# Kernel optimization log

Measured on AMD Instinct MI355X. Metric: run time of the kernel, lower is better.

Reference implementation:

```python
import jax, jax.numpy as jnp
import numpy as np

D_MODEL = 1024
PATCH = 16
HID = 256
VOCAB = 256

def setup_inputs() -> dict:
    key = jax.random.key(0)
    ks = jax.random.split(key, 12)
    B, N = 16, 512
    s = lambda *sh: 1.0 / np.sqrt(sh[-1])
    inp = {
        'latents': jax.random.normal(ks[0], (B, N, D_MODEL), dtype=jnp.float32),
        'target_bytes': jax.random.randint(ks[1], (B, N * PATCH), 0, VOCAB, dtype=jnp.int64),
        'W_proj': jax.random.normal(ks[2], (HID, D_MODEL), dtype=jnp.float32) * s(HID, D_MODEL),
        'b_proj': jnp.zeros((HID,), dtype=jnp.float32),
        'emb_table': jax.random.normal(ks[3], (VOCAB, HID), dtype=jnp.float32),
        'W_ih': jax.random.normal(ks[4], (3 * HID, 2 * HID), dtype=jnp.float32) * s(1, 2 * HID),
        'W_hh': jax.random.normal(ks[5], (3 * HID, HID), dtype=jnp.float32) * s(1, HID),
        'b_ih': jnp.zeros((3 * HID,), dtype=jnp.float32),
        'b_hh': jnp.zeros((3 * HID,), dtype=jnp.float32),
        'W_head': jax.random.normal(ks[6], (VOCAB, HID), dtype=jnp.float32) * s(VOCAB, HID),
        'b_head': jnp.zeros((VOCAB,), dtype=jnp.float32),
    }
    return inp

def _gru_scan(x_proj, W_hh, b_hh, h0):
    # x_proj: [T, BN, 3H] precomputed input projections (incl. b_ih)
    def step(h, xg):
        hg = h @ W_hh.T + b_hh                      # [BN, 3H]
        xr, xz, xn = jnp.split(xg, 3, axis=-1)
        hr, hz, hn = jnp.split(hg, 3, axis=-1)
        r = jax.nn.sigmoid(xr + hr)
        z = jax.nn.sigmoid(xz + hz)
        n = jnp.tanh(xn + r * hn)
        h_new = (1.0 - z) * n + z * h
        return h_new, h_new
    _, outs = jax.lax.scan(step, h0, x_proj)
    return outs                                      # [T, BN, H]

def reference(latents, target_bytes, W_proj, b_proj, emb_table, W_ih, W_hh, b_ih, b_hh, W_head, b_head):
    B, N, D = latents.shape
    BN = B * N
    latent_ctx = (latents.reshape(BN, D) @ W_proj.T + b_proj)        # [BN, H]
    targets = target_bytes.reshape(BN, PATCH)
    sos = jnp.zeros((BN, 1), dtype=targets.dtype)
    rnn_in_bytes = jnp.concatenate([sos, targets[:, :-1]], axis=1)   # [BN, P]
    emb = emb_table[rnn_in_bytes]                                    # [BN, P, H]
    lat_exp = jnp.broadcast_to(latent_ctx[:, None, :], (BN, PATCH, HID))
    rnn_input = jnp.concatenate([emb, lat_exp], axis=-1)             # [BN, P, 2H]
    x_proj = jnp.einsum('bpi,gi->bpg', rnn_input, W_ih) + b_ih       # [BN, P, 3H]
    h0 = jnp.zeros((BN, HID), dtype=latents.dtype)
    outs = _gru_scan(jnp.swapaxes(x_proj, 0, 1), W_hh, b_hh, h0)     # [P, BN, H]
    outs = jnp.swapaxes(outs, 0, 1)                                  # [BN, P, H]
    logits = jnp.einsum('bph,vh->bpv', outs, W_head) + b_head        # [BN, P, 256]
    return logits.reshape(B, N, PATCH, VOCAB)
```

## Files before the change

kernel.cpp:

```cpp
#include <hip/hip_runtime.h>
#include <math.h>

#define NSEQ 8192
#define PATCHL 16
#define HIDN 256
#define VOCABN 256

typedef __attribute__((ext_vector_type(4))) float f32x4;
typedef __attribute__((ext_vector_type(8))) short bf16x8;

__device__ __forceinline__ unsigned short f2bf(float f) {
    unsigned int x = __float_as_uint(f);
    unsigned int r = (x + 0x7fffu + ((x >> 16) & 1u)) >> 16;
    return (unsigned short)r;
}
__device__ __forceinline__ float bf2f(unsigned short b) {
    return __uint_as_float(((unsigned int)b) << 16);
}
__device__ __forceinline__ float sigf(float x)   { return 1.f / (1.f + __expf(-x)); }
__device__ __forceinline__ float tanhf_(float x) { return 2.f / (1.f + __expf(-2.f * x)) - 1.f; }

__global__ __launch_bounds__(256)
void pack_frag(const float* __restrict__ src, int ld, int col0, int nks,
               unsigned short* __restrict__ dst)
{
    const int g = blockIdx.x * 256 + threadIdx.x;
    const int lane = g & 63;
    const int ks = (g / 64) % nks;
    const int T  = g / (64 * nks);
    const float* s = src + (size_t)(T * 16 + (lane & 15)) * ld + col0 + ks * 32 + ((lane >> 4) & 3) * 8;
    unsigned int q[4];
#pragma unroll
    for (int j = 0; j < 4; j++) {
        unsigned int lo = f2bf(s[2 * j]);
        unsigned int hi = f2bf(s[2 * j + 1]);
        q[j] = lo | (hi << 16);
    }
    uint4 v; v.x = q[0]; v.y = q[1]; v.z = q[2]; v.w = q[3];
    *(uint4*)(dst + (size_t)g * 8) = v;
}

template<bool ASRC_BF16, int OUT_MODE>
__global__ __launch_bounds__(512)
void gemm_mfma(const void* __restrict__ Asrc, int lda,
               const unsigned short* __restrict__ bpack, int nks_total,
               const float* __restrict__ bias, void* __restrict__ Cdst, int ldc,
               int K)
{
    const int tid = threadIdx.x;
    const int w = tid >> 6, lane = tid & 63;
    const int l15 = lane & 15, kg = (lane >> 4) & 3;
    const int bm = blockIdx.x * 128, bn = blockIdx.y * 64;

    __shared__ unsigned short As[2][128 * 64];

    const int srow = tid >> 2;
    const int scol = (tid & 3) * 16;
    const int nkt = K / 64;

    f32x4 acc[4];
#pragma unroll
    for (int nt = 0; nt < 4; nt++) acc[nt] = 0.f;

    const int wb0 = srow * 128 + ((scol * 2) ^ ((srow & 7) << 4));
    const int wb1 = srow * 128 + ((scol * 2 + 16) ^ ((srow & 7) << 4));

#define STAGE(kt, buf) do {                                                         \
        const int gk = (kt) * 64 + scol;                                            \
        unsigned short tmp[16];                                                     \
        if (ASRC_BF16) {                                                            \
            const unsigned short* A = (const unsigned short*)Asrc;                  \
            *(uint4*)(tmp)     = *(const uint4*)(A + (size_t)(bm + srow) * lda + gk);      \
            *(uint4*)(tmp + 8) = *(const uint4*)(A + (size_t)(bm + srow) * lda + gk + 8);  \
        } else {                                                                    \
            const float* A = (const float*)Asrc;                                    \
            const float4 a0 = *(const float4*)(A + (size_t)(bm + srow) * lda + gk);       \
            const float4 a1 = *(const float4*)(A + (size_t)(bm + srow) * lda + gk + 4);   \
            const float4 a2 = *(const float4*)(A + (size_t)(bm + srow) * lda + gk + 8);   \
            const float4 a3 = *(const float4*)(A + (size_t)(bm + srow) * lda + gk + 12);  \
            tmp[0] = f2bf(a0.x);  tmp[1] = f2bf(a0.y);  tmp[2] = f2bf(a0.z);  tmp[3] = f2bf(a0.w);   \
            tmp[4] = f2bf(a1.x);  tmp[5] = f2bf(a1.y);  tmp[6] = f2bf(a1.z);  tmp[7] = f2bf(a1.w);   \
            tmp[8] = f2bf(a2.x);  tmp[9] = f2bf(a2.y);  tmp[10] = f2bf(a2.z); tmp[11] = f2bf(a2.w);  \
            tmp[12] = f2bf(a3.x); tmp[13] = f2bf(a3.y); tmp[14] = f2bf(a3.z); tmp[15] = f2bf(a3.w);  \
        }                                                                           \
        *(uint4*)((char*)As[buf] + wb0) = *(uint4*)tmp;                             \
        *(uint4*)((char*)As[buf] + wb1) = *(uint4*)(tmp + 8);                       \
    } while (0)

    STAGE(0, 0);
    __syncthreads();

    for (int kt = 0; kt < nkt; ++kt) {
        if (kt + 1 < nkt) STAGE(kt + 1, (kt + 1) & 1);
        const unsigned short* buf = As[kt & 1];
        const int row = w * 16 + l15;
#pragma unroll
        for (int ks = 0; ks < 2; ++ks) {
            const int bo = row * 128 + (((ks * 64) + kg * 16) ^ ((row & 7) << 4));
            const bf16x8 a = *(const bf16x8*)((const char*)buf + bo);
#pragma unroll
            for (int nt = 0; nt < 4; ++nt) {
                const int T = blockIdx.y * 4 + nt;
                const bf16x8 b = *(const bf16x8*)(bpack + (((size_t)T * nks_total + (kt * 2 + ks)) * 64 + lane) * 8);
                acc[nt] = __builtin_amdgcn_mfma_f32_16x16x32_bf16(a, b, acc[nt], 0, 0, 0);
            }
        }
        __syncthreads();
    }
#undef STAGE

#pragma unroll
    for (int nt = 0; nt < 4; ++nt) {
        const int n = bn + nt * 16 + l15;
        const float bv = bias ? bias[n] : 0.f;
#pragma unroll
        for (int rr = 0; rr < 4; ++rr) {
            const int m = bm + w * 16 + kg * 4 + rr;
            const float v = acc[nt][rr] + bv;
            if (OUT_MODE == 0)      ((float*)Cdst)[(size_t)m * ldc + n] = v;
            else if (OUT_MODE == 1) ((unsigned short*)Cdst)[(size_t)m * ldc + n] = f2bf(v);
            else                    ((unsigned short*)Cdst)[(size_t)m * 1024 + (n & 255) * 4 + (n >> 8)] = f2bf(v);
        }
    }
}

#define G4S 1032
__global__ __launch_bounds__(512)
void gru_scan_fused(const int* __restrict__ bytes,
                    const unsigned short* __restrict__ latg4,
                    const unsigned short* __restrict__ pmx4,
                    const unsigned short* __restrict__ wpack,
                    const float* __restrict__ b_hh,
                    unsigned short* __restrict__ hh,
                    int seq0)
{
    const int tid  = threadIdx.x;
    const int w    = tid >> 6;
    const int lane = tid & 63;
    const int l15  = lane & 15;
    const int kg   = (lane >> 4) & 3;
    const int s0l  = blockIdx.x * 16;
    const int s0g  = seq0 + s0l;

    __shared__ unsigned short PMs[16 * G4S];
    __shared__ unsigned short LG[16 * G4S];
    __shared__ unsigned short H[16 * 256];
    __shared__ int BYs[256];

    if (tid < 256) BYs[tid] = bytes[(size_t)s0g * PATCHL + tid];

#pragma unroll
    for (int j = 0; j < 4; ++j) {
        const int idx = j * 512 + tid;
        const int row = idx >> 7, col = idx & 127;
        *(uint4*)(LG + row * G4S + col * 8) =
            *(const uint4*)(latg4 + (size_t)(s0g + row) * 1024 + col * 8);
    }

    float bhr[2], bhz[2], bhn[2];
#pragma unroll
    for (int nt = 0; nt < 2; nt++) {
        const int u = w * 32 + nt * 16 + l15;
        bhr[nt] = b_hh[u]; bhz[nt] = b_hh[256 + u]; bhn[nt] = b_hh[512 + u];
    }

    float hreg[2][4];
#pragma unroll
    for (int nt = 0; nt < 2; nt++)
#pragma unroll
        for (int rr = 0; rr < 4; rr++) hreg[nt][rr] = 0.f;

    __syncthreads();

    for (int p = 0; p < PATCHL; ++p) {
#pragma unroll
        for (int j = 0; j < 4; ++j) {
            const int idx = j * 512 + tid;
            const int row = idx >> 7, col = idx & 127;
            const int bv = p ? BYs[row * PATCHL + p - 1] : 0;
            *(uint4*)(PMs + row * G4S + col * 8) =
                *(const uint4*)(pmx4 + (size_t)bv * 1024 + col * 8);
        }

        if (p) {
#pragma unroll
            for (int rj = 0; rj < 2; ++rj) {
                const int row = w * 2 + rj;
                const int boff = (lane * 8) ^ ((row & 7) << 4);
                const ushort4 v = *(const ushort4*)((const char*)(H + row * 256) + boff);
                *(ushort4*)(hh + ((size_t)(s0l + row) * PATCHL + (p - 1)) * 256 + lane * 4) = v;
            }
        }

        f32x4 accr[2], accz[2], accn[2];
#pragma unroll
        for (int nt = 0; nt < 2; nt++) { accr[nt] = 0.f; accz[nt] = 0.f; accn[nt] = 0.f; }
        if (p != 0) {
#pragma unroll
            for (int ks = 0; ks < 8; ++ks) {
                const int s = l15;
                const int off = (ks * 64 + kg * 16) ^ ((s & 7) << 4);
                const bf16x8 a = *(const bf16x8*)(H + s * 256 + (off >> 1));
#pragma unroll
                for (int nt = 0; nt < 2; nt++) {
                    const int tb = w * 2 + nt;
                    const bf16x8 br = *(const bf16x8*)(wpack + (((size_t)(tb)      * 8 + ks) * 64 + lane) * 8);
                    const bf16x8 bz = *(const bf16x8*)(wpack + (((size_t)(16 + tb) * 8 + ks) * 64 + lane) * 8);
                    const bf16x8 bn = *(const bf16x8*)(wpack + (((size_t)(32 + tb) * 8 + ks) * 64 + lane) * 8);
                    accr[nt] = __builtin_amdgcn_mfma_f32_16x16x32_bf16(a, br, accr[nt], 0, 0, 0);
                    accz[nt] = __builtin_amdgcn_mfma_f32_16x16x32_bf16(a, bz, accz[nt], 0, 0, 0);
                    accn[nt] = __builtin_amdgcn_mfma_f32_16x16x32_bf16(a, bn, accn[nt], 0, 0, 0);
                }
            }
        }
        __syncthreads();

#pragma unroll
        for (int nt = 0; nt < 2; nt++) {
            const int u = w * 32 + nt * 16 + l15;
#pragma unroll
            for (int rr = 0; rr < 4; rr++) {
                const int sl = kg * 4 + rr;
                const ushort4 pm4 = *(const ushort4*)(PMs + sl * G4S + u * 4);
                const ushort4 lg4 = *(const ushort4*)(LG  + sl * G4S + u * 4);
                const float xr = bf2f(lg4.x) + bf2f(pm4.x) + bhr[nt];
                const float xz = bf2f(lg4.y) + bf2f(pm4.y) + bhz[nt];
                const float xn = bf2f(lg4.z) + bf2f(pm4.z);
                const float r = sigf(xr + accr[nt][rr]);
                const float z = sigf(xz + accz[nt][rr]);
                const float n = tanhf_(xn + r * (accn[nt][rr] + bhn[nt]));
                const float hn_ = (1.f - z) * n + z * hreg[nt][rr];
                hreg[nt][rr] = hn_;
                const int bo = (2 * u) ^ ((sl & 7) << 4);
                H[sl * 256 + (bo >> 1)] = f2bf(hn_);
            }
        }
        __syncthreads();
    }

#pragma unroll
    for (int rj = 0; rj < 2; ++rj) {
        const int row = w * 2 + rj;
        const int boff = (lane * 8) ^ ((row & 7) << 4);
        const ushort4 v = *(const ushort4*)((const char*)(H + row * 256) + boff);
        *(ushort4*)(hh + ((size_t)(s0l + row) * PATCHL + (PATCHL - 1)) * 256 + lane * 4) = v;
    }
}

extern "C" void kernel_launch(void* const* d_in, const int* in_sizes, int n_in,
                              void* d_out, int out_size, void* d_ws, size_t ws_size,
                              hipStream_t stream)
{
    const float* latents = (const float*)d_in[0];
    const int*   tb      = (const int*)d_in[1];
    const float* W_proj  = (const float*)d_in[2];
    const float* b_proj  = (const float*)d_in[3];
    const float* emb     = (const float*)d_in[4];
    const float* W_ih    = (const float*)d_in[5];
    const float* W_hh    = (const float*)d_in[6];
    const float* b_ih    = (const float*)d_in[7];
    const float* b_hh    = (const float*)d_in[8];
    const float* W_head  = (const float*)d_in[9];
    const float* b_head  = (const float*)d_in[10];
    float* out = (float*)d_out;

    char* w = (char*)d_ws;
    unsigned short* latg4   = (unsigned short*)w;          w += (size_t)NSEQ * 1024 * 2;
    unsigned short* ctxb    = (unsigned short*)w;          w += (size_t)NSEQ * HIDN * 2;
    unsigned short* pmx4    = (unsigned short*)w;          w += 256 * 1024 * 2;
    unsigned short* bpack1  = (unsigned short*)w;          w += 16 * 32 * 64 * 8 * 2;
    unsigned short* bpack2  = (unsigned short*)w;          w += 48 * 8 * 64 * 8 * 2;
    unsigned short* bpack3  = (unsigned short*)w;          w += 48 * 8 * 64 * 8 * 2;
    unsigned short* wpackG  = (unsigned short*)w;          w += 48 * 8 * 64 * 8 * 2;
    unsigned short* bpackH  = (unsigned short*)w;          w += 16 * 8 * 64 * 8 * 2;
    unsigned short* hh_c    = (unsigned short*)w;
    const size_t fixed_bytes = (size_t)(w - (char*)d_ws);
    const size_t chunk_full  = (size_t)NSEQ * PATCHL * 256 * 2;

    int nch = 1;
    while (nch < 16 && fixed_bytes + chunk_full / nch > ws_size) nch <<= 1;
    const int SPC = NSEQ / nch;

    hipLaunchKernelGGL(pack_frag, dim3(128), dim3(256), 0, stream, W_proj, 1024, 0, 32, bpack1);
    hipLaunchKernelGGL(pack_frag, dim3(96),  dim3(256), 0, stream, W_ih,   512, 256, 8, bpack2);
    hipLaunchKernelGGL(pack_frag, dim3(96),  dim3(256), 0, stream, W_ih,   512, 0,   8, bpack3);
    hipLaunchKernelGGL(pack_frag, dim3(96),  dim3(256), 0, stream, W_hh,   256, 0,   8, wpackG);
    hipLaunchKernelGGL(pack_frag, dim3(32),  dim3(256), 0, stream, W_head, 256, 0,   8, bpackH);

    hipLaunchKernelGGL((gemm_mfma<false, 2>), dim3(2, 12), dim3(512), 0, stream,
                       emb, 256, bpack3, 8, nullptr, pmx4, 1024, 256);
    hipLaunchKernelGGL((gemm_mfma<false, 1>), dim3(NSEQ / 128, 4), dim3(512), 0, stream,
                       latents, 1024, bpack1, 32, b_proj, ctxb, 256, 1024);
    hipLaunchKernelGGL((gemm_mfma<true, 2>), dim3(NSEQ / 128, 12), dim3(512), 0, stream,
                       ctxb, 256, bpack2, 8, b_ih, latg4, 1024, 256);

    for (int c = 0; c < nch; ++c) {
        const int seq0 = c * SPC;
        hipLaunchKernelGGL(gru_scan_fused, dim3(SPC / 16), dim3(512), 0, stream,
                           tb, latg4, pmx4, wpackG, b_hh, hh_c, seq0);
        hipLaunchKernelGGL((gemm_mfma<true, 0>), dim3(SPC * PATCHL / 128, 4), dim3(512), 0, stream,
                           hh_c, 256, bpackH, 8, b_head,
                           out + (size_t)seq0 * PATCHL * VOCABN, 256, 256);
    }
}
```

Baseline: 343.7 us.

## Process 32 sequences per GRU block to reuse W_hh fragments across two M-tiles

Each GRU scan block now handles 32 sequences with 1024 threads instead of 16 with 512. Each wave computes 16 hidden units for both 16-row M tiles, so every W_hh fragment loaded from global memory feeds two MFMAs. This halves weight traffic per sequence in the recurrent step. In exchange, LDS per block roughly doubles to about 150KB, which limits a CU to one block, and there are fewer blocks per chunk.

Result: slower. 419.4 us (+22.0%).

```diff
diff --git a/kernel.cpp b/kernel.cpp
--- a/kernel.cpp
+++ b/kernel.cpp
@@ -125,7 +125,7 @@
 }
 
 #define G4S 1032
-__global__ __launch_bounds__(512)
+__global__ __launch_bounds__(1024)
 void gru_scan_fused(const int* __restrict__ bytes,
                     const unsigned short* __restrict__ latg4,
                     const unsigned short* __restrict__ pmx4,
@@ -139,43 +139,39 @@
     const int lane = tid & 63;
     const int l15  = lane & 15;
     const int kg   = (lane >> 4) & 3;
-    const int s0l  = blockIdx.x * 16;
+    const int s0l  = blockIdx.x * 32;
     const int s0g  = seq0 + s0l;
 
-    __shared__ unsigned short PMs[16 * G4S];
-    __shared__ unsigned short LG[16 * G4S];
-    __shared__ unsigned short H[16 * 256];
-    __shared__ int BYs[256];
-
-    if (tid < 256) BYs[tid] = bytes[(size_t)s0g * PATCHL + tid];
+    __shared__ unsigned short PMs[32 * G4S];
+    __shared__ unsigned short LG[32 * G4S];
+    __shared__ unsigned short H[32 * 256];
+    __shared__ int BYs[512];
+
+    if (tid < 512) BYs[tid] = bytes[(size_t)s0g * PATCHL + tid];
 
 #pragma unroll
     for (int j = 0; j < 4; ++j) {
-        const int idx = j * 512 + tid;
+        const int idx = j * 1024 + tid;
         const int row = idx >> 7, col = idx & 127;
         *(uint4*)(LG + row * G4S + col * 8) =
             *(const uint4*)(latg4 + (size_t)(s0g + row) * 1024 + col * 8);
     }
 
-    float bhr[2], bhz[2], bhn[2];
-#pragma unroll
-    for (int nt = 0; nt < 2; nt++) {
-        const int u = w * 32 + nt * 16 + l15;
-        bhr[nt] = b_hh[u]; bhz[nt] = b_hh[256 + u]; bhn[nt] = b_hh[512 + u];
-    }
+    const int u = w * 16 + l15;
+    const float bhr = b_hh[u], bhz = b_hh[256 + u], bhn = b_hh[512 + u];
 
     float hreg[2][4];
 #pragma unroll
-    for (int nt = 0; nt < 2; nt++)
-#pragma unroll
-        for (int rr = 0; rr < 4; rr++) hreg[nt][rr] = 0.f;
+    for (int mt = 0; mt < 2; mt++)
+#pragma unroll
+        for (int rr = 0; rr < 4; rr++) hreg[mt][rr] = 0.f;
 
     __syncthreads();
 
     for (int p = 0; p < PATCHL; ++p) {
 #pragma unroll
         for (int j = 0; j < 4; ++j) {
-            const int idx = j * 512 + tid;
+            const int idx = j * 1024 + tid;
             const int row = idx >> 7, col = idx & 127;
             const int bv = p ? BYs[row * PATCHL + p - 1] : 0;
             *(uint4*)(PMs + row * G4S + col * 8) =
@@ -194,47 +190,57 @@
 
         f32x4 accr[2], accz[2], accn[2];
 #pragma unroll
-        for (int nt = 0; nt < 2; nt++) { accr[nt] = 0.f; accz[nt] = 0.f; accn[nt] = 0.f; }
+        for (int mt = 0; mt < 2; mt++) { accr[mt] = 0.f; accz[mt] = 0.f; accn[mt] = 0.f; }
         if (p != 0) {
 #pragma unroll
-            for (int ks = 0; ks < 8; ++ks) {
-                const int s = l15;
-                const int off = (ks * 64 + kg * 16) ^ ((s & 7) << 4);
-                const bf16x8 a = *(const bf16x8*)(H + s * 256 + (off >> 1));
-#pragma unroll
-                for (int nt = 0; nt < 2; nt++) {
-                    const int tb = w * 2 + nt;
-                    const bf16x8 br = *(const bf16x8*)(wpack + (((size_t)(tb)      * 8 + ks) * 64 + lane) * 8);
-                    const bf16x8 bz = *(const bf16x8*)(wpack + (((size_t)(16 + tb) * 8 + ks) * 64 + lane) * 8);
-                    const bf16x8 bn = *(const bf16x8*)(wpack + (((size_t)(32 + tb) * 8 + ks) * 64 + lane) * 8);
-                    accr[nt] = __builtin_amdgcn_mfma_f32_16x16x32_bf16(a, br, accr[nt], 0, 0, 0);
-                    accz[nt] = __builtin_amdgcn_mfma_f32_16x16x32_bf16(a, bz, accz[nt], 0, 0, 0);
-                    accn[nt] = __builtin_amdgcn_mfma_f32_16x16x32_bf16(a, bn, accn[nt], 0, 0, 0);
+            for (int ksg = 0; ksg < 2; ++ksg) {
+                bf16x8 a[2][4];
+#pragma unroll
+                for (int mt = 0; mt < 2; ++mt)
+#pragma unroll
+                    for (int j = 0; j < 4; ++j) {
+                        const int s = mt * 16 + l15;
+                        const int off = ((ksg * 4 + j) * 64 + kg * 16) ^ ((s & 7) << 4);
+                        a[mt][j] = *(const bf16x8*)(H + s * 256 + (off >> 1));
+                    }
+#pragma unroll
+                for (int g = 0; g < 3; ++g) {
+                    const int T = g * 16 + w;
+                    bf16x8 B4[4];
+#pragma unroll
+                    for (int j = 0; j < 4; ++j)
+                        B4[j] = *(const bf16x8*)(wpack + (((size_t)T * 8 + ksg * 4 + j) * 64 + lane) * 8);
+#pragma unroll
+                    for (int j = 0; j < 4; ++j)
+#pragma unroll
+                        for (int mt = 0; mt < 2; ++mt) {
+                            if (g == 0)      accr[mt] = __builtin_amdgcn_mfma_f32_16x16x32_bf16(a[mt][j], B4[j], accr[mt], 0, 0, 0);
+                            else if (g == 1) accz[mt] = __builtin_amdgcn_mfma_f32_16x16x32_bf16(a[mt][j], B4[j], accz[mt], 0, 0, 0);
+                            else             accn[mt] = __builtin_amdgcn_mfma_f32_16x16x32_bf16(a[mt][j], B4[j], accn[mt], 0, 0, 0);
+                        }
                 }
             }
         }
         __syncthreads();
 
 #pragma unroll
-        for (int nt = 0; nt < 2; nt++) {
-            const int u = w * 32 + nt * 16 + l15;
+        for (int mt = 0; mt < 2; mt++)
 #pragma unroll
             for (int rr = 0; rr < 4; rr++) {
-                const int sl = kg * 4 + rr;
+                const int sl = mt * 16 + kg * 4 + rr;
                 const ushort4 pm4 = *(const ushort4*)(PMs + sl * G4S + u * 4);
                 const ushort4 lg4 = *(const ushort4*)(LG  + sl * G4S + u * 4);
-                const float xr = bf2f(lg4.x) + bf2f(pm4.x) + bhr[nt];
-                const float xz = bf2f(lg4.y) + bf2f(pm4.y) + bhz[nt];
+                const float xr = bf2f(lg4.x) + bf2f(pm4.x) + bhr;
+                const float xz = bf2f(lg4.y) + bf2f(pm4.y) + bhz;
                 const float xn = bf2f(lg4.z) + bf2f(pm4.z);
-                const float r = sigf(xr + accr[nt][rr]);
-                const float z = sigf(xz + accz[nt][rr]);
-                const float n = tanhf_(xn + r * (accn[nt][rr] + bhn[nt]));
-                const float hn_ = (1.f - z) * n + z * hreg[nt][rr];
-                hreg[nt][rr] = hn_;
+                const float r = sigf(xr + accr[mt][rr]);
+                const float z = sigf(xz + accz[mt][rr]);
+                const float n = tanhf_(xn + r * (accn[mt][rr] + bhn));
+                const float hn_ = (1.f - z) * n + z * hreg[mt][rr];
+                hreg[mt][rr] = hn_;
                 const int bo = (2 * u) ^ ((sl & 7) << 4);
                 H[sl * 256 + (bo >> 1)] = f2bf(hn_);
             }
-        }
         __syncthreads();
     }
 
@@ -296,7 +302,7 @@
 
     for (int c = 0; c < nch; ++c) {
         const int seq0 = c * SPC;
-        hipLaunchKernelGGL(gru_scan_fused, dim3(SPC / 16), dim3(512), 0, stream,
+        hipLaunchKernelGGL(gru_scan_fused, dim3(SPC / 32), dim3(1024), 0, stream,
                            tb, latg4, pmx4, wpackG, b_hh, hh_c, seq0);
         hipLaunchKernelGGL((gemm_mfma<true, 0>), dim3(SPC * PATCHL / 128, 4), dim3(512), 0, stream,
                            hh_c, 256, bpackH, 8, b_head,
```

## Double-buffer hidden state and prefetch next step's input projections in GRU scan

Applied to the files above, without the earlier changes.

The GRU scan kernel now keeps two hidden-state buffers in shared memory and two buffers for the gathered per-byte input projections. The projections for step p+1 are prefetched while step p computes, which removes one of the two block barriers per timestep. The cost is extra shared memory (a second 16x1032 bf16 buffer plus a second H buffer), which may lower occupancy. The per-step barrier chain is also now the only thing ordering the buffer reuse.

Result: slower. 373.2 us (+8.6%).

```diff
diff --git a/kernel.cpp b/kernel.cpp
--- a/kernel.cpp
+++ b/kernel.cpp
@@ -142,9 +142,10 @@
     const int s0l  = blockIdx.x * 16;
     const int s0g  = seq0 + s0l;
 
-    __shared__ unsigned short PMs[16 * G4S];
+    __shared__ unsigned short PMs[2][16 * G4S];
+    __shared__ unsigned short H0[16 * 256];
+    __shared__ unsigned short H1[16 * 256];
     __shared__ unsigned short LG[16 * G4S];
-    __shared__ unsigned short H[16 * 256];
     __shared__ int BYs[256];
 
     if (tid < 256) BYs[tid] = bytes[(size_t)s0g * PATCHL + tid];
@@ -157,6 +158,14 @@
             *(const uint4*)(latg4 + (size_t)(s0g + row) * 1024 + col * 8);
     }
 
+#pragma unroll
+    for (int j = 0; j < 4; ++j) {
+        const int idx = j * 512 + tid;
+        const int row = idx >> 7, col = idx & 127;
+        *(uint4*)(PMs[0] + row * G4S + col * 8) =
+            *(const uint4*)(pmx4 + col * 8);
+    }
+
     float bhr[2], bhz[2], bhn[2];
 #pragma unroll
     for (int nt = 0; nt < 2; nt++) {
@@ -170,16 +179,21 @@
 #pragma unroll
         for (int rr = 0; rr < 4; rr++) hreg[nt][rr] = 0.f;
 
+    unsigned short* Hcur = H0;
+    unsigned short* Hnxt = H1;
+
     __syncthreads();
 
     for (int p = 0; p < PATCHL; ++p) {
-#pragma unroll
-        for (int j = 0; j < 4; ++j) {
-            const int idx = j * 512 + tid;
-            const int row = idx >> 7, col = idx & 127;
-            const int bv = p ? BYs[row * PATCHL + p - 1] : 0;
-            *(uint4*)(PMs + row * G4S + col * 8) =
-                *(const uint4*)(pmx4 + (size_t)bv * 1024 + col * 8);
+        if (p + 1 < PATCHL) {
+#pragma unroll
+            for (int j = 0; j < 4; ++j) {
+                const int idx = j * 512 + tid;
+                const int row = idx >> 7, col = idx & 127;
+                const int bv = BYs[row * PATCHL + p];
+                *(uint4*)(PMs[(p + 1) & 1] + row * G4S + col * 8) =
+                    *(const uint4*)(pmx4 + (size_t)bv * 1024 + col * 8);
+            }
         }
 
         if (p) {
@@ -187,7 +201,7 @@
             for (int rj = 0; rj < 2; ++rj) {
                 const int row = w * 2 + rj;
                 const int boff = (lane * 8) ^ ((row & 7) << 4);
-                const ushort4 v = *(const ushort4*)((const char*)(H + row * 256) + boff);
+                const ushort4 v = *(const ushort4*)((const char*)(Hcur + row * 256) + boff);
                 *(ushort4*)(hh + ((size_t)(s0l + row) * PATCHL + (p - 1)) * 256 + lane * 4) = v;
             }
         }
@@ -198,9 +212,8 @@
         if (p != 0) {
 #pragma unroll
             for (int ks = 0; ks < 8; ++ks) {
-                const int s = l15;
-                const int off = (ks * 64 + kg * 16) ^ ((s & 7) << 4);
-                const bf16x8 a = *(const bf16x8*)(H + s * 256 + (off >> 1));
+                const int off = (ks * 64 + kg * 16) ^ ((l15 & 7) << 4);
+                const bf16x8 a = *(const bf16x8*)(Hcur + l15 * 256 + (off >> 1));
 #pragma unroll
                 for (int nt = 0; nt < 2; nt++) {
                     const int tb = w * 2 + nt;
@@ -213,15 +226,15 @@
                 }
             }
         }
-        __syncthreads();
-
+
+        const unsigned short* PMc = PMs[p & 1];
 #pragma unroll
         for (int nt = 0; nt < 2; nt++) {
             const int u = w * 32 + nt * 16 + l15;
 #pragma unroll
             for (int rr = 0; rr < 4; rr++) {
                 const int sl = kg * 4 + rr;
-                const ushort4 pm4 = *(const ushort4*)(PMs + sl * G4S + u * 4);
+                const ushort4 pm4 = *(const ushort4*)(PMc + sl * G4S + u * 4);
                 const ushort4 lg4 = *(const ushort4*)(LG  + sl * G4S + u * 4);
                 const float xr = bf2f(lg4.x) + bf2f(pm4.x) + bhr[nt];
                 const float xz = bf2f(lg4.y) + bf2f(pm4.y) + bhz[nt];
@@ -232,17 +245,18 @@
                 const float hn_ = (1.f - z) * n + z * hreg[nt][rr];
                 hreg[nt][rr] = hn_;
                 const int bo = (2 * u) ^ ((sl & 7) << 4);
-                H[sl * 256 + (bo >> 1)] = f2bf(hn_);
+                Hnxt[sl * 256 + (bo >> 1)] = f2bf(hn_);
             }
         }
         __syncthreads();
+        unsigned short* t_ = Hcur; Hcur = Hnxt; Hnxt = t_;
     }
 
 #pragma unroll
     for (int rj = 0; rj < 2; ++rj) {
         const int row = w * 2 + rj;
         const int boff = (lane * 8) ^ ((row & 7) << 4);
-        const ushort4 v = *(const ushort4*)((const char*)(H + row * 256) + boff);
+        const ushort4 v = *(const ushort4*)((const char*)(Hcur + row * 256) + boff);
         *(ushort4*)(hh + ((size_t)(s0l + row) * PATCHL + (PATCHL - 1)) * 256 + lane * 4) = v;
     }
 }
```
